# Kernel tuning notes

Measured on AMD Instinct MI355X. Metric: run time of the kernel, lower is better.

## Reference

```python
import jax, jax.numpy as jnp
import numpy as np

N_NODES = 10000
N_EDGES = 320000
NHID = 128


def setup_inputs() -> dict:
    key = jax.random.key(0)
    k1, k2, k3, k4 = jax.random.split(key, 4)
    h = jax.random.normal(k1, (N_NODES, NHID), dtype=jnp.float32)
    # GraphConv weight (Glorot-ish scale) and bias
    W = jax.random.normal(k2, (NHID, NHID), dtype=jnp.float32) * (1.0 / np.sqrt(NHID))
    b = jnp.zeros((NHID,), dtype=jnp.float32)
    edge_src = jax.random.randint(k3, (N_EDGES,), 0, N_NODES, dtype=jnp.int32)
    edge_dst = jax.random.randint(k4, (N_EDGES,), 0, N_NODES, dtype=jnp.int32)
    return {"h": h, "W": W, "b": b, "edge_src": edge_src, "edge_dst": edge_dst}


def reference(h, W, b, edge_src, edge_dst):
    """DOMINANT Structure_Decoder forward (eval mode, dropout is identity).

    GraphConv(nhid, nhid, norm='none'): since in_feats == out_feats, DGL applies
    the weight first, then sum-aggregates source->dst messages, then adds bias.
    Then: relu -> (dropout skipped in eval) -> dense x @ x.T reconstruction.
    """
    n = h.shape[0]
    hw = h @ W                                            # [N, nhid]
    agg = jax.ops.segment_sum(hw[edge_src], edge_dst, num_segments=n)  # SpMM: sum over in-edges
    x = jax.nn.relu(agg + b)                              # [N, nhid]
    return x @ x.T                                        # [N, N] reconstructed adjacency
```

## Files before the change

### kernel.cpp

```cpp
#include <hip/hip_runtime.h>
#include <hip/hip_bf16.h>
#include <stdint.h>

#define N_NODES 10000
#define N_EDGES 320000
#define NHID    128
#define N_PAD   10112

typedef unsigned short u16;
typedef float f32x4 __attribute__((ext_vector_type(4)));
typedef short bf16x8 __attribute__((ext_vector_type(8)));

__global__ __launch_bounds__(256) void scatter_kernel(
    const float* __restrict__ h,
    const int* __restrict__ esrc,
    const int* __restrict__ edst,
    float* __restrict__ agg) {
  const int total = N_EDGES * NHID;
  const int stride = gridDim.x * blockDim.x;
  for (int i = blockIdx.x * blockDim.x + threadIdx.x; i < total; i += stride) {
    const int e = i >> 7;
    const int c = i & (NHID - 1);
    const float v = h[(size_t)esrc[e] * NHID + c];
    atomicAdd(&agg[(size_t)edst[e] * NHID + c], v);
  }
}

__global__ __launch_bounds__(256) void gemm_relu_split(
    const float* __restrict__ agg,
    const float* __restrict__ W,
    const float* __restrict__ b,
    u16* __restrict__ xhi,
    u16* __restrict__ xlo) {
  __shared__ float Ws[NHID * NHID];
  __shared__ float As[32 * NHID];
  const int tid = threadIdx.x;
  const int row0 = blockIdx.x * 32;

  for (int i = tid; i < NHID * NHID / 4; i += 256)
    reinterpret_cast<float4*>(Ws)[i] = reinterpret_cast<const float4*>(W)[i];
  for (int i = tid; i < 32 * NHID / 4; i += 256) {
    const int r = row0 + (i >> 5);
    float4 v = make_float4(0.f, 0.f, 0.f, 0.f);
    if (r < N_NODES) v = reinterpret_cast<const float4*>(agg)[(size_t)row0 * 32 + i];
    reinterpret_cast<float4*>(As)[i] = v;
  }
  __syncthreads();

  const int col = tid & (NHID - 1);
  const int half = tid >> 7;
  const float bias = b[col];

  for (int r = half; r < 32; r += 2) {
    float acc = 0.f;
#pragma unroll
    for (int k = 0; k < NHID; ++k)
      acc = fmaf(As[r * NHID + k], Ws[k * NHID + col], acc);
    const int grow = row0 + r;
    if (grow < N_PAD) {
      float x = 0.f;
      if (grow < N_NODES) x = fmaxf(acc + bias, 0.f);
      const uint32_t u = __builtin_bit_cast(uint32_t, x);
      const uint32_t hibits = (u + 0x7FFFu + ((u >> 16) & 1u)) & 0xFFFF0000u;
      const float hif = __builtin_bit_cast(float, hibits);
      const float lof = x - hif;
      const uint32_t ul = __builtin_bit_cast(uint32_t, lof);
      const uint32_t lobits = (ul + 0x7FFFu + ((ul >> 16) & 1u)) & 0xFFFF0000u;
      const size_t idx = (size_t)grow * NHID + col;
      xhi[idx] = (u16)(hibits >> 16);
      xlo[idx] = (u16)(lobits >> 16);
    }
  }
}

__global__ __launch_bounds__(256) void xxt_kernel(
    const u16* __restrict__ xhi,
    const u16* __restrict__ xlo,
    float* __restrict__ out) {
  const int bj = blockIdx.x;
  const int bi = blockIdx.y;
  const int lane = threadIdx.x & 63;
  const int wid = threadIdx.x >> 6;
  const int wm = (wid >> 1) * 64;
  const int wn = (wid & 1) * 64;

  const int arow = bi * 128 + wm + (lane & 15);
  const int brow = bj * 128 + wn + (lane & 15);
  const int koff = (lane >> 4) * 8;

  const u16* pah = xhi + (size_t)arow * NHID + koff;
  const u16* pal = xlo + (size_t)arow * NHID + koff;
  const u16* pbh = xhi + (size_t)brow * NHID + koff;
  const u16* pbl = xlo + (size_t)brow * NHID + koff;

  f32x4 acc[4][4];
#pragma unroll
  for (int mi = 0; mi < 4; ++mi)
#pragma unroll
    for (int ni = 0; ni < 4; ++ni)
      acc[mi][ni] = (f32x4){0.f, 0.f, 0.f, 0.f};

#pragma unroll
  for (int ks = 0; ks < 4; ++ks) {
    bf16x8 ah[4], al[4], bh[4], bl[4];
#pragma unroll
    for (int mi = 0; mi < 4; ++mi) {
      ah[mi] = *reinterpret_cast<const bf16x8*>(pah + (size_t)mi * 16 * NHID + ks * 32);
      al[mi] = *reinterpret_cast<const bf16x8*>(pal + (size_t)mi * 16 * NHID + ks * 32);
      bh[mi] = *reinterpret_cast<const bf16x8*>(pbh + (size_t)mi * 16 * NHID + ks * 32);
      bl[mi] = *reinterpret_cast<const bf16x8*>(pbl + (size_t)mi * 16 * NHID + ks * 32);
    }
#pragma unroll
    for (int mi = 0; mi < 4; ++mi)
#pragma unroll
      for (int ni = 0; ni < 4; ++ni) {
        acc[mi][ni] = __builtin_amdgcn_mfma_f32_16x16x32_bf16(ah[mi], bh[ni], acc[mi][ni], 0, 0, 0);
        acc[mi][ni] = __builtin_amdgcn_mfma_f32_16x16x32_bf16(al[mi], bh[ni], acc[mi][ni], 0, 0, 0);
        acc[mi][ni] = __builtin_amdgcn_mfma_f32_16x16x32_bf16(ah[mi], bl[ni], acc[mi][ni], 0, 0, 0);
      }
  }

  const int crow0 = bi * 128 + wm + (lane >> 4) * 4;
  const int ccol0 = bj * 128 + wn + (lane & 15);
#pragma unroll
  for (int mi = 0; mi < 4; ++mi) {
#pragma unroll
    for (int ni = 0; ni < 4; ++ni) {
      const int col = ccol0 + ni * 16;
      if (col < N_NODES) {
#pragma unroll
        for (int r = 0; r < 4; ++r) {
          const int row = crow0 + mi * 16 + r;
          if (row < N_NODES)
            out[(size_t)row * N_NODES + col] = acc[mi][ni][r];
        }
      }
    }
  }
}

extern "C" void kernel_launch(void* const* d_in, const int* in_sizes, int n_in,
                              void* d_out, int out_size, void* d_ws, size_t ws_size,
                              hipStream_t stream) {
  const float* h   = (const float*)d_in[0];
  const float* W   = (const float*)d_in[1];
  const float* b   = (const float*)d_in[2];
  const int* esrc  = (const int*)d_in[3];
  const int* edst  = (const int*)d_in[4];
  float* out = (float*)d_out;

  char* ws = (char*)d_ws;
  float* agg = (float*)ws;
  u16* xhi = (u16*)(ws + 5120000);
  u16* xlo = (u16*)(ws + 5120000 + 2588672);

  hipMemsetAsync(agg, 0, (size_t)N_NODES * NHID * sizeof(float), stream);

  scatter_kernel<<<4096, 256, 0, stream>>>(h, esrc, edst, agg);

  gemm_relu_split<<<N_PAD / 32, 256, 0, stream>>>(agg, W, b, xhi, xlo);

  dim3 grid(79, 79);
  xxt_kernel<<<grid, 256, 0, stream>>>(xhi, xlo, out);
}
```

Baseline: 706.3 us.

## Replace atomic edge scatter with CSR build and per-node gather; remap XXT tiles per XCD

Drops the per-element atomicAdd scatter of source rows into agg. In its place, a CSR layout is built on the GPU with a histogram, a single-block scan and a fill pass, then a gather kernel sums neighbour rows for each destination node in registers. This removes roughly 41M float atomics, at the cost of three small extra launches, a serial one-block scan and an extra integer atomic per edge. The XXT kernel also remaps block IDs so that consecutive tiles land on the same XCD, which should improve L2 reuse of the xhi/xlo rows. A redundant bounds check in the GEMM is removed as well.

```diff
diff --git a/kernel.cpp b/kernel.cpp
--- a/kernel.cpp
+++ b/kernel.cpp
@@ -11,19 +11,85 @@
 typedef float f32x4 __attribute__((ext_vector_type(4)));
 typedef short bf16x8 __attribute__((ext_vector_type(8)));
 
-__global__ __launch_bounds__(256) void scatter_kernel(
+__global__ __launch_bounds__(256) void hist_kernel(
+    const int* __restrict__ edst, int* __restrict__ cnt) {
+  const int e = blockIdx.x * 256 + threadIdx.x;
+  if (e < N_EDGES) atomicAdd(&cnt[edst[e]], 1);
+}
+
+__global__ __launch_bounds__(1024) void scan_kernel(
+    const int* __restrict__ cnt, int* __restrict__ offs) {
+  __shared__ int wsum[16];
+  __shared__ int carry_s;
+  const int tid = threadIdx.x;
+  const int lane = tid & 63;
+  const int wv = tid >> 6;
+  if (tid == 0) carry_s = 0;
+  __syncthreads();
+  for (int base = 0; base < N_NODES; base += 1024) {
+    const int i = base + tid;
+    const int v = (i < N_NODES) ? cnt[i] : 0;
+    int s = v;
+#pragma unroll
+    for (int d = 1; d < 64; d <<= 1) {
+      int t = __shfl_up(s, d);
+      if (lane >= d) s += t;
+    }
+    if (lane == 63) wsum[wv] = s;
+    __syncthreads();
+    if (tid < 16) {
+      int t = wsum[tid];
+#pragma unroll
+      for (int d = 1; d < 16; d <<= 1) {
+        int u = __shfl_up(t, d);
+        if (tid >= d) t += u;
+      }
+      wsum[tid] = t;
+    }
+    __syncthreads();
+    const int carry = carry_s;
+    const int pre = (wv == 0 ? 0 : wsum[wv - 1]);
+    if (i < N_NODES) offs[i] = carry + pre + (s - v);
+    __syncthreads();
+    if (tid == 0) carry_s = carry + wsum[15];
+    __syncthreads();
+  }
+  if (tid == 0) offs[N_NODES] = N_EDGES;
+}
+
+__global__ __launch_bounds__(256) void fill_kernel(
+    const int* __restrict__ esrc, const int* __restrict__ edst,
+    const int* __restrict__ offs, int* __restrict__ cursor,
+    int* __restrict__ srcs) {
+  const int e = blockIdx.x * 256 + threadIdx.x;
+  if (e < N_EDGES) {
+    const int d = edst[e];
+    const int p = atomicAdd(&cursor[d], 1);
+    srcs[offs[d] + p] = esrc[e];
+  }
+}
+
+__global__ __launch_bounds__(128) void gather_kernel(
     const float* __restrict__ h,
-    const int* __restrict__ esrc,
-    const int* __restrict__ edst,
+    const int* __restrict__ offs,
+    const int* __restrict__ srcs,
     float* __restrict__ agg) {
-  const int total = N_EDGES * NHID;
-  const int stride = gridDim.x * blockDim.x;
-  for (int i = blockIdx.x * blockDim.x + threadIdx.x; i < total; i += stride) {
-    const int e = i >> 7;
-    const int c = i & (NHID - 1);
-    const float v = h[(size_t)esrc[e] * NHID + c];
-    atomicAdd(&agg[(size_t)edst[e] * NHID + c], v);
-  }
+  __shared__ int sl[256];
+  const int n = blockIdx.x;
+  const int c = threadIdx.x;
+  const int beg = offs[n];
+  const int deg = offs[n + 1] - beg;
+  float acc = 0.f;
+  for (int j0 = 0; j0 < deg; j0 += 256) {
+    const int m = min(deg - j0, 256);
+    for (int j = c; j < m; j += 128) sl[j] = srcs[beg + j0 + j];
+    __syncthreads();
+#pragma unroll 4
+    for (int j = 0; j < m; ++j)
+      acc += h[(size_t)sl[j] * NHID + c];
+    __syncthreads();
+  }
+  agg[(size_t)n * NHID + c] = acc;
 }
 
 __global__ __launch_bounds__(256) void gemm_relu_split(
@@ -57,19 +123,17 @@
     for (int k = 0; k < NHID; ++k)
       acc = fmaf(As[r * NHID + k], Ws[k * NHID + col], acc);
     const int grow = row0 + r;
-    if (grow < N_PAD) {
-      float x = 0.f;
-      if (grow < N_NODES) x = fmaxf(acc + bias, 0.f);
-      const uint32_t u = __builtin_bit_cast(uint32_t, x);
-      const uint32_t hibits = (u + 0x7FFFu + ((u >> 16) & 1u)) & 0xFFFF0000u;
-      const float hif = __builtin_bit_cast(float, hibits);
-      const float lof = x - hif;
-      const uint32_t ul = __builtin_bit_cast(uint32_t, lof);
-      const uint32_t lobits = (ul + 0x7FFFu + ((ul >> 16) & 1u)) & 0xFFFF0000u;
-      const size_t idx = (size_t)grow * NHID + col;
-      xhi[idx] = (u16)(hibits >> 16);
-      xlo[idx] = (u16)(lobits >> 16);
-    }
+    float x = 0.f;
+    if (grow < N_NODES) x = fmaxf(acc + bias, 0.f);
+    const uint32_t u = __builtin_bit_cast(uint32_t, x);
+    const uint32_t hibits = (u + 0x7FFFu + ((u >> 16) & 1u)) & 0xFFFF0000u;
+    const float hif = __builtin_bit_cast(float, hibits);
+    const float lof = x - hif;
+    const uint32_t ul = __builtin_bit_cast(uint32_t, lof);
+    const uint32_t lobits = (ul + 0x7FFFu + ((ul >> 16) & 1u)) & 0xFFFF0000u;
+    const size_t idx = (size_t)grow * NHID + col;
+    xhi[idx] = (u16)(hibits >> 16);
+    xlo[idx] = (u16)(lobits >> 16);
   }
 }
 
@@ -77,8 +141,15 @@
     const u16* __restrict__ xhi,
     const u16* __restrict__ xlo,
     float* __restrict__ out) {
-  const int bj = blockIdx.x;
-  const int bi = blockIdx.y;
+  const int nwg = 79 * 79;
+  const int flat = blockIdx.y * 79 + blockIdx.x;
+  const int q = nwg >> 3, r = nwg & 7;
+  const int xcd = flat & 7;
+  const int jj = flat >> 3;
+  const int nid = (xcd < r ? xcd * (q + 1) : r * (q + 1) + (xcd - r) * q) + jj;
+  const int bi = nid / 79;
+  const int bj = nid % 79;
+
   const int lane = threadIdx.x & 63;
   const int wid = threadIdx.x >> 6;
   const int wm = (wid >> 1) * 64;
@@ -150,13 +221,20 @@
   float* out = (float*)d_out;
 
   char* ws = (char*)d_ws;
-  float* agg = (float*)ws;
-  u16* xhi = (u16*)(ws + 5120000);
-  u16* xlo = (u16*)(ws + 5120000 + 2588672);
-
-  hipMemsetAsync(agg, 0, (size_t)N_NODES * NHID * sizeof(float), stream);
-
-  scatter_kernel<<<4096, 256, 0, stream>>>(h, esrc, edst, agg);
+  float* agg  = (float*)(ws);
+  u16* xhi    = (u16*)(ws + 5120000);
+  u16* xlo    = (u16*)(ws + 7708672);
+  int* cnt    = (int*)(ws + 10297344);
+  int* cursor = (int*)(ws + 10337344);
+  int* offs   = (int*)(ws + 10377344);
+  int* srcs   = (int*)(ws + 10417360);
+
+  hipMemsetAsync(cnt, 0, 80000, stream);
+
+  hist_kernel<<<(N_EDGES + 255) / 256, 256, 0, stream>>>(edst, cnt);
+  scan_kernel<<<1, 1024, 0, stream>>>(cnt, offs);
+  fill_kernel<<<(N_EDGES + 255) / 256, 256, 0, stream>>>(esrc, edst, offs, cursor, srcs);
+  gather_kernel<<<N_NODES, 128, 0, stream>>>(h, offs, srcs, agg);
 
   gemm_relu_split<<<N_PAD / 32, 256, 0, stream>>>(agg, W, b, xhi, xlo);
 
```

Measured after the change: 661.6 us. 1.07x faster.
